# Optimization experiments

Measured on AMD Instinct MI355X. Metric: run time of the kernel, lower is better.

The kernel has to match this reference:

```python
import jax, jax.numpy as jnp
import numpy as np

NEG_SLOPE = 0.2  # PyG GATConv default


def _gat_layer(x, src, dst, W, a_s, a_d, b, num_nodes):
    H, C = a_s.shape
    h = (x @ W).reshape(num_nodes, H, C)                     # [N,H,C]
    alpha_src = jnp.einsum('nhc,hc->nh', h, a_s)             # [N,H]
    alpha_dst = jnp.einsum('nhc,hc->nh', h, a_d)             # [N,H]
    e = jax.nn.leaky_relu(alpha_src[src] + alpha_dst[dst], NEG_SLOPE)  # [E,H]
    # segment softmax over incoming edges of each destination node
    m = jax.lax.stop_gradient(jax.ops.segment_max(e, dst, num_segments=num_nodes))
    e = jnp.exp(e - m[dst])
    den = jax.ops.segment_sum(e, dst, num_segments=num_nodes)
    alpha = e / den[dst]                                     # [E,H]
    msg = h[src] * alpha[:, :, None]                         # [E,H,C]
    out = jax.ops.segment_sum(msg, dst, num_segments=num_nodes)
    return out.reshape(num_nodes, H * C) + b


def setup_inputs() -> dict:
    key = jax.random.key(0)
    ks = jax.random.split(key, 10)
    N, E, D, H, C = 100000, 1600000, 128, 4, 32
    s = 1.0 / np.sqrt(D)
    return {
        'x': jax.random.normal(ks[0], (N, D), jnp.float32),
        'edge_index': jax.random.randint(ks[1], (2, E), 0, N, jnp.int64),
        'W1': jax.random.normal(ks[2], (D, H * C), jnp.float32) * s,
        'a_src1': jax.random.normal(ks[3], (H, C), jnp.float32) * s,
        'a_dst1': jax.random.normal(ks[4], (H, C), jnp.float32) * s,
        'b1': jnp.zeros((H * C,), jnp.float32),
        'W2': jax.random.normal(ks[5], (H * C, H * C), jnp.float32) * s,
        'a_src2': jax.random.normal(ks[6], (H, C), jnp.float32) * s,
        'a_dst2': jax.random.normal(ks[7], (H, C), jnp.float32) * s,
        'b2': jnp.zeros((H * C,), jnp.float32),
    }


def reference(x, edge_index, W1, a_src1, a_dst1, b1, W2, a_src2, a_dst2, b2):
    N = x.shape[0]
    loop = jnp.arange(N, dtype=edge_index.dtype)  # PyG add_self_loops=True
    src = jnp.concatenate([edge_index[0], loop])
    dst = jnp.concatenate([edge_index[1], loop])
    h = _gat_layer(x, src, dst, W1, a_src1, a_dst1, b1, N)
    h = jax.nn.relu(h)
    h = _gat_layer(h, src, dst, W2, a_src2, a_dst2, b2, N)
    return jax.nn.relu(h)
```

## Files before the change

kernel.cpp:

```cpp
#include <hip/hip_runtime.h>
#include <cstdint>
#include <cstddef>

#define NEG_SLOPE 0.2f
#define BIN_SHIFT 9
#define BCAP 16384
#define LOG2E 1.4426950408889634f
#define ROWB 272

typedef short bf16x8 __attribute__((ext_vector_type(8)));
typedef float f32x4 __attribute__((ext_vector_type(4)));

#if __has_builtin(__builtin_amdgcn_exp2f)
#define EXP2(x) __builtin_amdgcn_exp2f(x)
#else
#define EXP2(x) exp2f(x)
#endif

static __device__ __forceinline__ unsigned short bf16r(float f) {
    unsigned u = __float_as_uint(f);
    return (unsigned short)((u + 0x7fffu + ((u >> 16) & 1u)) >> 16);
}
static __device__ __forceinline__ float bfu_lo(unsigned u) { return __uint_as_float(u << 16); }
static __device__ __forceinline__ float bfu_hi(unsigned u) { return __uint_as_float(u & 0xffff0000u); }

__global__ __launch_bounds__(256) void wprep_k(const float* __restrict__ W1, const float* __restrict__ W2,
                                               unsigned short* __restrict__ Wh1, unsigned short* __restrict__ Wl1,
                                               unsigned short* __restrict__ Wh2, unsigned short* __restrict__ Wl2,
                                               int* __restrict__ bcnt) {
    if (blockIdx.x == 0) bcnt[threadIdx.x] = 0;
    int t = blockIdx.x * 256 + threadIdx.x;
    const float* W;
    unsigned short *Wh, *Wl;
    int idx;
    if (t < 16384) { W = W1; Wh = Wh1; Wl = Wl1; idx = t; }
    else           { W = W2; Wh = Wh2; Wl = Wl2; idx = t - 16384; }
    int c = idx >> 7;
    int k = idx & 127;
    float w = W[(size_t)k * 128 + c];
    unsigned short h = bf16r(w);
    float lo = w - __uint_as_float((unsigned)h << 16);
    Wh[c * 128 + k] = h;
    Wl[c * 128 + k] = bf16r(lo);
}

__global__ __launch_bounds__(256) void bin_k(const int* __restrict__ srcI, const int* __restrict__ dstI,
                                             int E, int N, int K, int* __restrict__ bcnt,
                                             int2* __restrict__ tmpE) {
    __shared__ int hist[256];
    __shared__ int lbase[256];
    const int t = threadIdx.x;
    const int M = E + N;
    const int chunk0 = blockIdx.x * 2048;
    hist[t] = 0;
    __syncthreads();

    int s[8], d[8], b[8];
#pragma unroll
    for (int j = 0; j < 8; ++j) {
        int i = chunk0 + t + j * 256;
        b[j] = -1;
        if (i < M) {
            int ss, dd;
            if (i < E) { ss = srcI[i]; dd = dstI[i]; }
            else       { ss = i - E;  dd = ss; }
            if ((unsigned)dd < (unsigned)N && (unsigned)ss < (unsigned)N) {
                s[j] = ss; d[j] = dd; b[j] = dd >> BIN_SHIFT;
                atomicAdd(&hist[b[j]], 1);
            }
        }
    }
    __syncthreads();
    if (t < K) {
        int c = hist[t];
        lbase[t] = (c > 0) ? atomicAdd(&bcnt[t], c) : 0;
    }
    hist[t] = 0;
    __syncthreads();
#pragma unroll
    for (int j = 0; j < 8; ++j) {
        if (b[j] >= 0) {
            int r = atomicAdd(&hist[b[j]], 1);
            int pos = lbase[b[j]] + r;
            if (pos < BCAP) tmpE[(size_t)b[j] * BCAP + pos] = make_int2(s[j], d[j]);
        }
    }
}

__global__ __launch_bounds__(256) void scatter_csr_k(const int2* __restrict__ tmpE,
                                                     const int* __restrict__ bcnt,
                                                     int* __restrict__ rowptr,
                                                     int* __restrict__ colOff,
                                                     int N, int K) {
    __shared__ int pre[256];
    __shared__ int cur[512];
    __shared__ int ss[256];
    const int t = threadIdx.x;
    const int b = blockIdx.x;

    int bc = (t < K) ? min(bcnt[t], BCAP) : 0;
    pre[t] = bc;
    __syncthreads();
    for (int off = 1; off < 256; off <<= 1) {
        int v = (t >= off) ? pre[t - off] : 0;
        __syncthreads();
        pre[t] += v;
        __syncthreads();
    }
    const int base_b = (b == 0) ? 0 : pre[b - 1];
    const int cnt_b  = pre[b] - base_b;
    if (b == K - 1 && t == 0) rowptr[N] = pre[K - 1];

    const int nlo = b << BIN_SHIFT;
    const int nhi = min(nlo + (1 << BIN_SHIFT), N);
    const int nn  = nhi - nlo;
    const int2* te = tmpE + (size_t)b * BCAP;

    cur[t] = 0;
    cur[t + 256] = 0;
    __syncthreads();
    for (int i = t; i < cnt_b; i += 256) atomicAdd(&cur[te[i].y - nlo], 1);
    __syncthreads();

    int v0 = cur[2 * t], v1 = cur[2 * t + 1];
    ss[t] = v0 + v1;
    __syncthreads();
    for (int off = 1; off < 256; off <<= 1) {
        int v = (t >= off) ? ss[t - off] : 0;
        __syncthreads();
        ss[t] += v;
        __syncthreads();
    }
    int e0 = (t == 0) ? 0 : ss[t - 1];
    int e1 = e0 + v0;
    if (2 * t < nn)     rowptr[nlo + 2 * t]     = base_b + e0;
    if (2 * t + 1 < nn) rowptr[nlo + 2 * t + 1] = base_b + e1;
    cur[2 * t] = e0;
    cur[2 * t + 1] = e1;
    __syncthreads();

    for (int i = t; i < cnt_b; i += 256) {
        int2 sd = te[i];
        int r = atomicAdd(&cur[sd.y - nlo], 1);
        colOff[base_b + r] = sd.x * ROWB;
    }
}

__global__ __launch_bounds__(256) void gemm_mfma_k(const float* __restrict__ X,
                                                   const unsigned short* __restrict__ Wh,
                                                   const unsigned short* __restrict__ Wl,
                                                   const float* __restrict__ a_s,
                                                   const float* __restrict__ a_d,
                                                   char* __restrict__ Hout,
                                                   float* __restrict__ adst,
                                                   int N) {
    __shared__ __align__(16) unsigned short hstage[4][32][132];
    const int tid = threadIdx.x;
    const int wid = tid >> 6;
    const int l   = tid & 63;
    const int l15 = l & 15;
    const int lh  = l >> 4;
    const int waveRow = blockIdx.x * 128 + wid * 32;
    if (waveRow >= N) return;

    f32x4 acc[2][8];
#pragma unroll
    for (int m = 0; m < 2; ++m)
#pragma unroll
        for (int f = 0; f < 8; ++f)
#pragma unroll
            for (int c = 0; c < 4; ++c) acc[m][f][c] = 0.f;

    const int r0 = waveRow + l15;
    const int r1 = waveRow + 16 + l15;
    const size_t xoff0 = (size_t)min(r0, N - 1) * 128;
    const size_t xoff1 = (size_t)min(r1, N - 1) * 128;
    const int kb = lh * 8;

#pragma unroll
    for (int ks = 0; ks < 4; ++ks) {
        bf16x8 ah[2], al[2];
#pragma unroll
        for (int m = 0; m < 2; ++m) {
            const float* xp = X + (m ? xoff1 : xoff0) + ks * 32 + kb;
            float4 v0 = *(const float4*)xp;
            float4 v1 = *(const float4*)(xp + 4);
            float xs[8] = {v0.x, v0.y, v0.z, v0.w, v1.x, v1.y, v1.z, v1.w};
#pragma unroll
            for (int j = 0; j < 8; ++j) {
                unsigned short h = bf16r(xs[j]);
                float hf = __uint_as_float((unsigned)h << 16);
                ah[m][j] = (short)h;
                al[m][j] = (short)bf16r(xs[j] - hf);
            }
        }
        const unsigned short* wb  = Wh + (size_t)l15 * 128 + ks * 32 + kb;
        const unsigned short* wbl = Wl + (size_t)l15 * 128 + ks * 32 + kb;
#pragma unroll
        for (int f = 0; f < 8; ++f) {
            bf16x8 wh = *(const bf16x8*)(wb + f * 2048);
            bf16x8 wl = *(const bf16x8*)(wbl + f * 2048);
#pragma unroll
            for (int m = 0; m < 2; ++m) {
                acc[m][f] = __builtin_amdgcn_mfma_f32_16x16x32_bf16(ah[m], wh, acc[m][f], 0, 0, 0);
                acc[m][f] = __builtin_amdgcn_mfma_f32_16x16x32_bf16(al[m], wh, acc[m][f], 0, 0, 0);
                acc[m][f] = __builtin_amdgcn_mfma_f32_16x16x32_bf16(ah[m], wl, acc[m][f], 0, 0, 0);
            }
        }
    }

    float asf[8], adf[8];
#pragma unroll
    for (int f = 0; f < 8; ++f) {
        asf[f] = a_s[f * 16 + l15];
        adf[f] = a_d[f * 16 + l15];
    }
    const int q = l15;
#pragma unroll
    for (int m = 0; m < 2; ++m) {
#pragma unroll
        for (int r = 0; r < 4; ++r) {
            float ps[4] = {0.f, 0.f, 0.f, 0.f};
            float pd[4] = {0.f, 0.f, 0.f, 0.f};
#pragma unroll
            for (int f = 0; f < 8; ++f) {
                float v = acc[m][f][r];
                ps[f >> 1] = fmaf(v, asf[f], ps[f >> 1]);
                pd[f >> 1] = fmaf(v, adf[f], pd[f >> 1]);
                hstage[wid][m * 16 + lh * 4 + r][f * 16 + l15] = bf16r(v);
            }
#pragma unroll
            for (int mask = 1; mask < 16; mask <<= 1) {
#pragma unroll
                for (int h = 0; h < 4; ++h) {
                    ps[h] += __shfl_xor(ps[h], mask);
                    pd[h] += __shfl_xor(pd[h], mask);
                }
            }
            int row = waveRow + m * 16 + lh * 4 + r;
            if (q < 8 && row < N) {
                float v0 = (q & 1) ? ps[1] : ps[0];
                float v1 = (q & 1) ? ps[3] : ps[2];
                float vs = (q & 2) ? v1 : v0;
                float w0 = (q & 1) ? pd[1] : pd[0];
                float w1 = (q & 1) ? pd[3] : pd[2];
                float vd = (q & 2) ? w1 : w0;
                if (q < 4) *(float*)(Hout + (size_t)row * ROWB + 256 + q * 4) = vs * LOG2E;
                else       adst[row * 4 + (q - 4)] = vd * LOG2E;
            }
        }
    }

#pragma unroll
    for (int it = 0; it < 8; ++it) {
        int row = it * 4 + lh;
        const unsigned short* hp = &hstage[wid][row][l15 * 8];
        uint2 aa = *(const uint2*)hp;
        uint2 bb = *(const uint2*)(hp + 4);
        int grow = waveRow + row;
        if (grow < N) {
            uint4 o;
            o.x = aa.x; o.y = aa.y; o.z = bb.x; o.w = bb.y;
            *(uint4*)(Hout + (size_t)grow * ROWB + l15 * 16) = o;
        }
    }
}

__global__ __launch_bounds__(256) void aggregate_k(const char* __restrict__ Hb,
                                                   const float* __restrict__ adst,
                                                   const int* __restrict__ rowptr,
                                                   const int* __restrict__ colOff,
                                                   const float* __restrict__ bias,
                                                   float* __restrict__ out, int N) {
    int wave = (blockIdx.x * 256 + threadIdx.x) >> 6;
    int lane = threadIdx.x & 63;
    if (wave >= N) return;
    const int n = wave;
    const int c0 = lane * 2;
    const int head = c0 >> 5;
    const float adh = adst[n * 4 + head];
    const int hoff = c0 * 2;
    const int aoff = 256 + head * 4;

    int b = __builtin_amdgcn_readfirstlane(rowptr[n]);
    int e = __builtin_amdgcn_readfirstlane(rowptr[n + 1]);
    float acc0 = 0.f, acc1 = 0.f, sw = 0.f;
    int p = b;
    for (; p + 8 <= e; p += 8) {
        int off[8];
#pragma unroll
        for (int j = 0; j < 8; ++j) off[j] = colOff[p + j];
        float a[8];
#pragma unroll
        for (int j = 0; j < 8; ++j) a[j] = *(const float*)(Hb + off[j] + aoff);
        unsigned hu[8];
#pragma unroll
        for (int j = 0; j < 8; ++j) hu[j] = *(const unsigned*)(Hb + off[j] + hoff);
#pragma unroll
        for (int j = 0; j < 8; ++j) {
            float x = a[j] + adh;
            float w = EXP2(fmaxf(x, NEG_SLOPE * x));
            sw += w;
            acc0 = fmaf(w, bfu_lo(hu[j]), acc0);
            acc1 = fmaf(w, bfu_hi(hu[j]), acc1);
        }
    }
    for (; p < e; ++p) {
        int off = colOff[p];
        float x = *(const float*)(Hb + off + aoff) + adh;
        unsigned u = *(const unsigned*)(Hb + off + hoff);
        float w = EXP2(fmaxf(x, NEG_SLOPE * x));
        sw += w;
        acc0 = fmaf(w, bfu_lo(u), acc0);
        acc1 = fmaf(w, bfu_hi(u), acc1);
    }
    float inv = 1.f / sw;
    float o0 = fmaxf(acc0 * inv + bias[c0], 0.f);
    float o1 = fmaxf(acc1 * inv + bias[c0 + 1], 0.f);
    *(float2*)&out[(size_t)n * 128 + c0] = make_float2(o0, o1);
}


extern "C" void kernel_launch(void* const* d_in, const int* in_sizes, int n_in,
                              void* d_out, int out_size, void* d_ws, size_t ws_size,
                              hipStream_t stream) {
    const float* X   = (const float*)d_in[0];
    const int*   EI  = (const int*)d_in[1];
    const float* W1  = (const float*)d_in[2];
    const float* as1 = (const float*)d_in[3];
    const float* ad1 = (const float*)d_in[4];
    const float* b1  = (const float*)d_in[5];
    const float* W2  = (const float*)d_in[6];
    const float* as2 = (const float*)d_in[7];
    const float* ad2 = (const float*)d_in[8];
    const float* b2  = (const float*)d_in[9];

    const int N = in_sizes[0] / 128;
    const int E = in_sizes[1] / 2;
    const int M = E + N;
    const int K = (N + (1 << BIN_SHIFT) - 1) >> BIN_SHIFT;
    const int* srcI = EI;
    const int* dstI = EI + E;

    char* w = (char*)d_ws;
    auto alloc = [&](size_t bytes) {
        char* p = w;
        w += (bytes + 255) & ~(size_t)255;
        return p;
    };
    char*  Hbuf   = (char*)alloc((size_t)N * ROWB);
    float* adst   = (float*)alloc((size_t)N * 4 * 4);
    int*   rowptr = (int*)alloc((size_t)(N + 1) * 4);
    int*   colOff = (int*)alloc((size_t)M * 4);
    int2*  tmpE   = (int2*)alloc((size_t)K * BCAP * 8);
    int*   bcnt   = (int*)alloc(256 * 4);
    unsigned short* Wt1h = (unsigned short*)alloc(128 * 128 * 2);
    unsigned short* Wt1l = (unsigned short*)alloc(128 * 128 * 2);
    unsigned short* Wt2h = (unsigned short*)alloc(128 * 128 * 2);
    unsigned short* Wt2l = (unsigned short*)alloc(128 * 128 * 2);

    const int gemmBlocks = (N + 127) / 128;

    wprep_k<<<128, 256, 0, stream>>>(W1, W2, Wt1h, Wt1l, Wt2h, Wt2l, bcnt);
    bin_k<<<(M + 2047) / 2048, 256, 0, stream>>>(srcI, dstI, E, N, K, bcnt, tmpE);
    scatter_csr_k<<<K, 256, 0, stream>>>(tmpE, bcnt, rowptr, colOff, N, K);

    float* out = (float*)d_out;

    gemm_mfma_k<<<gemmBlocks, 256, 0, stream>>>(X, Wt1h, Wt1l, as1, ad1, Hbuf, adst, N);
    aggregate_k<<<((size_t)N * 64 + 255) / 256, 256, 0, stream>>>(Hbuf, adst, rowptr, colOff, b1, out, N);
    gemm_mfma_k<<<gemmBlocks, 256, 0, stream>>>(out, Wt2h, Wt2l, as2, ad2, Hbuf, adst, N);
    aggregate_k<<<((size_t)N * 64 + 255) / 256, 256, 0, stream>>>(Hbuf, adst, rowptr, colOff, b2, out, N);
}
```

Before: 425.5 us.

## Split H rows and alpha_src, pack binned edges, pre-swizzle weights, unify tail loop

Node feature rows become dense 256-byte bf16 rows, and the source attention logits move to a separate array, so gathers in aggregation index with a power-of-two stride. Binned edges are packed into a single 32-bit word (source shifted, low 9 bits of destination), which halves the temporary traffic, and binning blocks now handle twice as many edges. Weights are pre-swizzled into MFMA fragment order so each lane reads one contiguous 16-byte chunk. The aggregation tail is merged into the 8-wide loop using clamped indices and masked weights, which adds some redundant loads in exchange for one uniform loop. The packing assumes source indices below 2^22, and the split layout costs an extra gather per edge from a separate array.

```diff
diff --git a/kernel.cpp b/kernel.cpp
--- a/kernel.cpp
+++ b/kernel.cpp
@@ -6,7 +6,6 @@
 #define BIN_SHIFT 9
 #define BCAP 16384
 #define LOG2E 1.4426950408889634f
-#define ROWB 272
 
 typedef short bf16x8 __attribute__((ext_vector_type(8)));
 typedef float f32x4 __attribute__((ext_vector_type(4)));
@@ -40,24 +39,25 @@
     float w = W[(size_t)k * 128 + c];
     unsigned short h = bf16r(w);
     float lo = w - __uint_as_float((unsigned)h << 16);
-    Wh[c * 128 + k] = h;
-    Wl[c * 128 + k] = bf16r(lo);
+    int dst = (k >> 5) * 4096 + (c >> 4) * 512 + (((k >> 3) & 3) * 16 + (c & 15)) * 8 + (k & 7);
+    Wh[dst] = h;
+    Wl[dst] = bf16r(lo);
 }
 
 __global__ __launch_bounds__(256) void bin_k(const int* __restrict__ srcI, const int* __restrict__ dstI,
                                              int E, int N, int K, int* __restrict__ bcnt,
-                                             int2* __restrict__ tmpE) {
+                                             int* __restrict__ tmpE) {
     __shared__ int hist[256];
     __shared__ int lbase[256];
     const int t = threadIdx.x;
     const int M = E + N;
-    const int chunk0 = blockIdx.x * 2048;
+    const int chunk0 = blockIdx.x * 4096;
     hist[t] = 0;
     __syncthreads();
 
-    int s[8], d[8], b[8];
-#pragma unroll
-    for (int j = 0; j < 8; ++j) {
+    int s[16], d[16], b[16];
+#pragma unroll
+    for (int j = 0; j < 16; ++j) {
         int i = chunk0 + t + j * 256;
         b[j] = -1;
         if (i < M) {
@@ -78,16 +78,16 @@
     hist[t] = 0;
     __syncthreads();
 #pragma unroll
-    for (int j = 0; j < 8; ++j) {
+    for (int j = 0; j < 16; ++j) {
         if (b[j] >= 0) {
             int r = atomicAdd(&hist[b[j]], 1);
             int pos = lbase[b[j]] + r;
-            if (pos < BCAP) tmpE[(size_t)b[j] * BCAP + pos] = make_int2(s[j], d[j]);
-        }
-    }
-}
-
-__global__ __launch_bounds__(256) void scatter_csr_k(const int2* __restrict__ tmpE,
+            if (pos < BCAP) tmpE[(size_t)b[j] * BCAP + pos] = (s[j] << 9) | (d[j] & 511);
+        }
+    }
+}
+
+__global__ __launch_bounds__(256) void scatter_csr_k(const int* __restrict__ tmpE,
                                                      const int* __restrict__ bcnt,
                                                      int* __restrict__ rowptr,
                                                      int* __restrict__ colOff,
@@ -114,12 +114,12 @@
     const int nlo = b << BIN_SHIFT;
     const int nhi = min(nlo + (1 << BIN_SHIFT), N);
     const int nn  = nhi - nlo;
-    const int2* te = tmpE + (size_t)b * BCAP;
+    const int* te = tmpE + (size_t)b * BCAP;
 
     cur[t] = 0;
     cur[t + 256] = 0;
     __syncthreads();
-    for (int i = t; i < cnt_b; i += 256) atomicAdd(&cur[te[i].y - nlo], 1);
+    for (int i = t; i < cnt_b; i += 256) atomicAdd(&cur[te[i] & 511], 1);
     __syncthreads();
 
     int v0 = cur[2 * t], v1 = cur[2 * t + 1];
@@ -140,9 +140,9 @@
     __syncthreads();
 
     for (int i = t; i < cnt_b; i += 256) {
-        int2 sd = te[i];
-        int r = atomicAdd(&cur[sd.y - nlo], 1);
-        colOff[base_b + r] = sd.x * ROWB;
+        int v = te[i];
+        int r = atomicAdd(&cur[v & 511], 1);
+        colOff[base_b + r] = ((unsigned)v >> 9) << 8;
     }
 }
 
@@ -151,7 +151,8 @@
                                                    const unsigned short* __restrict__ Wl,
                                                    const float* __restrict__ a_s,
                                                    const float* __restrict__ a_d,
-                                                   char* __restrict__ Hout,
+                                                   unsigned short* __restrict__ Hout,
+                                                   float* __restrict__ asrc,
                                                    float* __restrict__ adst,
                                                    int N) {
     __shared__ __align__(16) unsigned short hstage[4][32][132];
@@ -194,12 +195,12 @@
                 al[m][j] = (short)bf16r(xs[j] - hf);
             }
         }
-        const unsigned short* wb  = Wh + (size_t)l15 * 128 + ks * 32 + kb;
-        const unsigned short* wbl = Wl + (size_t)l15 * 128 + ks * 32 + kb;
+        const unsigned short* wbh = Wh + ks * 4096 + l * 8;
+        const unsigned short* wbl = Wl + ks * 4096 + l * 8;
 #pragma unroll
         for (int f = 0; f < 8; ++f) {
-            bf16x8 wh = *(const bf16x8*)(wb + f * 2048);
-            bf16x8 wl = *(const bf16x8*)(wbl + f * 2048);
+            bf16x8 wh = *(const bf16x8*)(wbh + f * 512);
+            bf16x8 wl = *(const bf16x8*)(wbl + f * 512);
 #pragma unroll
             for (int m = 0; m < 2; ++m) {
                 acc[m][f] = __builtin_amdgcn_mfma_f32_16x16x32_bf16(ah[m], wh, acc[m][f], 0, 0, 0);
@@ -245,7 +246,7 @@
                 float w0 = (q & 1) ? pd[1] : pd[0];
                 float w1 = (q & 1) ? pd[3] : pd[2];
                 float vd = (q & 2) ? w1 : w0;
-                if (q < 4) *(float*)(Hout + (size_t)row * ROWB + 256 + q * 4) = vs * LOG2E;
+                if (q < 4) asrc[row * 4 + q] = vs * LOG2E;
                 else       adst[row * 4 + (q - 4)] = vd * LOG2E;
             }
         }
@@ -261,12 +262,13 @@
         if (grow < N) {
             uint4 o;
             o.x = aa.x; o.y = aa.y; o.z = bb.x; o.w = bb.y;
-            *(uint4*)(Hout + (size_t)grow * ROWB + l15 * 16) = o;
-        }
-    }
-}
-
-__global__ __launch_bounds__(256) void aggregate_k(const char* __restrict__ Hb,
+            *(uint4*)&Hout[(size_t)grow * 128 + l15 * 8] = o;
+        }
+    }
+}
+
+__global__ __launch_bounds__(256) void aggregate_k(const unsigned short* __restrict__ Hbuf,
+                                                   const float* __restrict__ asrc,
                                                    const float* __restrict__ adst,
                                                    const int* __restrict__ rowptr,
                                                    const int* __restrict__ colOff,
@@ -279,40 +281,32 @@
     const int c0 = lane * 2;
     const int head = c0 >> 5;
     const float adh = adst[n * 4 + head];
+    const char* Hb = (const char*)Hbuf;
+    const char* As = (const char*)asrc;
     const int hoff = c0 * 2;
-    const int aoff = 256 + head * 4;
+    const int aoff = head * 4;
 
     int b = __builtin_amdgcn_readfirstlane(rowptr[n]);
     int e = __builtin_amdgcn_readfirstlane(rowptr[n + 1]);
     float acc0 = 0.f, acc1 = 0.f, sw = 0.f;
-    int p = b;
-    for (; p + 8 <= e; p += 8) {
+    for (int p = b; p < e; p += 8) {
         int off[8];
 #pragma unroll
-        for (int j = 0; j < 8; ++j) off[j] = colOff[p + j];
+        for (int j = 0; j < 8; ++j) off[j] = colOff[min(p + j, e - 1)];
         float a[8];
 #pragma unroll
-        for (int j = 0; j < 8; ++j) a[j] = *(const float*)(Hb + off[j] + aoff);
+        for (int j = 0; j < 8; ++j) a[j] = *(const float*)(As + (off[j] >> 4) + aoff);
         unsigned hu[8];
 #pragma unroll
         for (int j = 0; j < 8; ++j) hu[j] = *(const unsigned*)(Hb + off[j] + hoff);
 #pragma unroll
         for (int j = 0; j < 8; ++j) {
             float x = a[j] + adh;
-            float w = EXP2(fmaxf(x, NEG_SLOPE * x));
+            float w = (p + j < e) ? EXP2(fmaxf(x, NEG_SLOPE * x)) : 0.f;
             sw += w;
             acc0 = fmaf(w, bfu_lo(hu[j]), acc0);
             acc1 = fmaf(w, bfu_hi(hu[j]), acc1);
         }
-    }
-    for (; p < e; ++p) {
-        int off = colOff[p];
-        float x = *(const float*)(Hb + off + aoff) + adh;
-        unsigned u = *(const unsigned*)(Hb + off + hoff);
-        float w = EXP2(fmaxf(x, NEG_SLOPE * x));
-        sw += w;
-        acc0 = fmaf(w, bfu_lo(u), acc0);
-        acc1 = fmaf(w, bfu_hi(u), acc1);
     }
     float inv = 1.f / sw;
     float o0 = fmaxf(acc0 * inv + bias[c0], 0.f);
@@ -348,11 +342,12 @@
         w += (bytes + 255) & ~(size_t)255;
         return p;
     };
-    char*  Hbuf   = (char*)alloc((size_t)N * ROWB);
+    unsigned short* Hbuf = (unsigned short*)alloc((size_t)N * 128 * 2);
+    float* asrc   = (float*)alloc((size_t)N * 4 * 4);
     float* adst   = (float*)alloc((size_t)N * 4 * 4);
     int*   rowptr = (int*)alloc((size_t)(N + 1) * 4);
     int*   colOff = (int*)alloc((size_t)M * 4);
-    int2*  tmpE   = (int2*)alloc((size_t)K * BCAP * 8);
+    int*   tmpE   = (int*)alloc((size_t)K * BCAP * 4);
     int*   bcnt   = (int*)alloc(256 * 4);
     unsigned short* Wt1h = (unsigned short*)alloc(128 * 128 * 2);
     unsigned short* Wt1l = (unsigned short*)alloc(128 * 128 * 2);
@@ -360,15 +355,13 @@
     unsigned short* Wt2l = (unsigned short*)alloc(128 * 128 * 2);
 
     const int gemmBlocks = (N + 127) / 128;
+    float* out = (float*)d_out;
 
     wprep_k<<<128, 256, 0, stream>>>(W1, W2, Wt1h, Wt1l, Wt2h, Wt2l, bcnt);
-    bin_k<<<(M + 2047) / 2048, 256, 0, stream>>>(srcI, dstI, E, N, K, bcnt, tmpE);
+    bin_k<<<(M + 4095) / 4096, 256, 0, stream>>>(srcI, dstI, E, N, K, bcnt, tmpE);
     scatter_csr_k<<<K, 256, 0, stream>>>(tmpE, bcnt, rowptr, colOff, N, K);
-
-    float* out = (float*)d_out;
-
-    gemm_mfma_k<<<gemmBlocks, 256, 0, stream>>>(X, Wt1h, Wt1l, as1, ad1, Hbuf, adst, N);
-    aggregate_k<<<((size_t)N * 64 + 255) / 256, 256, 0, stream>>>(Hbuf, adst, rowptr, colOff, b1, out, N);
-    gemm_mfma_k<<<gemmBlocks, 256, 0, stream>>>(out, Wt2h, Wt2l, as2, ad2, Hbuf, adst, N);
-    aggregate_k<<<((size_t)N * 64 + 255) / 256, 256, 0, stream>>>(Hbuf, adst, rowptr, colOff, b2, out, N);
-}
+    gemm_mfma_k<<<gemmBlocks, 256, 0, stream>>>(X, Wt1h, Wt1l, as1, ad1, Hbuf, asrc, adst, N);
+    aggregate_k<<<((size_t)N * 64 + 255) / 256, 256, 0, stream>>>(Hbuf, asrc, adst, rowptr, colOff, b1, out, N);
+    gemm_mfma_k<<<gemmBlocks, 256, 0, stream>>>(out, Wt2h, Wt2l, as2, ad2, Hbuf, asrc, adst, N);
+    aggregate_k<<<((size_t)N * 64 + 255) / 256, 256, 0, stream>>>(Hbuf, asrc, adst, rowptr, colOff, b2, out, N);
+}
```

New measurement: 378.6 us. -11.0%, faster.
